# Performance work log

Measured on AMD Instinct MI355X. Metric: run time of the kernel, lower is better.

## Reference

```python
import jax, jax.numpy as jnp
import numpy as np

ALPHA = 3.0
NNODES, DIM, K = 8192, 64, 32


def setup_inputs() -> dict:
    key = jax.random.key(0)
    ks = jax.random.split(key, 8)
    return {
        "idx": jnp.arange(NNODES, dtype=jnp.int64) if jax.config.jax_enable_x64 else jnp.arange(NNODES, dtype=jnp.int32),
        "emb1": jax.random.normal(ks[0], (NNODES, DIM), dtype=jnp.float32),
        "emb2": jax.random.normal(ks[1], (NNODES, DIM), dtype=jnp.float32),
        "lin1_w": jax.random.normal(ks[2], (DIM, DIM), dtype=jnp.float32) * 0.1,
        "lin1_b": jax.random.normal(ks[3], (DIM,), dtype=jnp.float32) * 0.1,
        "lin2_w": jax.random.normal(ks[4], (DIM, DIM), dtype=jnp.float32) * 0.1,
        "lin2_b": jax.random.normal(ks[5], (DIM,), dtype=jnp.float32) * 0.1,
        "noise": jax.random.uniform(ks[6], (NNODES, NNODES), dtype=jnp.float32),
        "k": K,
    }


def reference(idx, emb1, emb2, lin1_w, lin1_b, lin2_w, lin2_b, noise, k):
    # gather node embeddings, project, tanh(alpha * .)
    nodevec1 = jnp.tanh(ALPHA * (emb1[idx] @ lin1_w.T + lin1_b))  # [N, D]
    nodevec2 = jnp.tanh(ALPHA * (emb2[idx] @ lin2_w.T + lin2_b))  # [N, D]
    # antisymmetric bilinear score
    a = nodevec1 @ nodevec2.T - nodevec2 @ nodevec1.T             # [N, N]
    adj = jax.nn.relu(jnp.tanh(ALPHA * a))                         # [N, N]
    n = adj.shape[0]
    # topk per row with uniform tie-break noise (torch: adj + rand*0.01)
    _, t1 = jax.lax.top_k(adj + noise * 0.01, k)                   # [N, k] int
    rows = jnp.arange(n)[:, None]                                  # [N, 1]
    mask = jnp.zeros((n, n), dtype=adj.dtype).at[rows, t1].set(1.0)
    adj = adj * mask + jnp.eye(n, dtype=adj.dtype)
    return adj
```

## Files before the change

kernel.cpp:

```cpp
#include <hip/hip_runtime.h>

#define NN 8192
#define DD 64
#define CC 128
#define XCLAMP 7.99881172180175781f

__device__ __forceinline__ float guard(float v) {
    asm volatile("" : "+v"(v));
    return v;
}

__device__ __forceinline__ float xla_tanhf(float x) {
    float xc = fminf(fmaxf(x, -XCLAMP), XCLAMP);
    float x2 = xc * xc;
    float p = fmaf(x2, -2.76076847742355e-16f, 2.00018790482477e-13f);
    p = fmaf(x2, p, -8.60467152213735e-11f);
    p = fmaf(x2, p, 5.12229709037114e-08f);
    p = fmaf(x2, p, 1.48572235717979e-05f);
    p = fmaf(x2, p, 6.37261928875436e-04f);
    p = fmaf(x2, p, 4.89352455891786e-03f);
    p = xc * p;
    float q = fmaf(x2, 1.19825839466702e-06f, 1.18534705686654e-04f);
    q = fmaf(x2, q, 2.26843463243900e-03f);
    q = fmaf(x2, q, 4.89352518554385e-03f);
    float r = p / q;
    return (fabsf(x) < 0.0004f) ? x : r;
}

__device__ __forceinline__ float score_of(float a, float nz) {
    float adj = fmaxf(xla_tanhf(3.0f * a), 0.0f);
    float m = guard(0.01f * nz);
    return adj + m;
}

__global__ __launch_bounds__(256) void k1_nodevec(
    const int* __restrict__ idx,
    const float* __restrict__ emb1, const float* __restrict__ emb2,
    const float* __restrict__ w1, const float* __restrict__ b1,
    const float* __restrict__ w2, const float* __restrict__ b2,
    float* __restrict__ Wt)
{
    __shared__ float sw1[64 * 65], sw2[64 * 65];
    __shared__ float sb1[64], sb2[64];
    __shared__ float se1[4][64], se2[4][64];
    int t = threadIdx.x;
    for (int i = t; i < 4096; i += 256) {
        int r = i >> 6, c = i & 63;
        sw1[r * 65 + c] = w1[i];
        sw2[r * 65 + c] = w2[i];
    }
    if (t < 64) { sb1[t] = b1[t]; sb2[t] = b2[t]; }
    int nl = t >> 6, d = t & 63;
    int n = blockIdx.x * 4 + nl;
    bool is64 = (idx[1] == 0);
    int g = (is64 ? idx[2 * n] : idx[n]) & 8191;
    se1[nl][d] = emb1[g * 64 + d];
    se2[nl][d] = emb2[g * 64 + d];
    __syncthreads();
    float z1 = 0.0f, z2 = 0.0f;
#pragma unroll 16
    for (int q = 0; q < 64; ++q) {
        z1 = fmaf(se1[nl][q], sw1[d * 65 + q], z1);
        z2 = fmaf(se2[nl][q], sw2[d * 65 + q], z2);
    }
    z1 = 3.0f * guard(z1 + sb1[d]);
    z2 = 3.0f * guard(z2 + sb2[d]);
    Wt[(size_t)d * NN + n]        = xla_tanhf(z1);
    Wt[(size_t)(64 + d) * NN + n] = xla_tanhf(z2);
}

__global__ __launch_bounds__(256) void k_init(
    float* __restrict__ listVal, int* __restrict__ listIdx)
{
    int i = blockIdx.x * 256 + threadIdx.x;
    listVal[i] = -1.0f;
    listIdx[i] = -1;
}

__global__ __launch_bounds__(512) void k2p_pairscore(
    const float* __restrict__ Wt, const float* __restrict__ noise,
    float* __restrict__ Sc)
{
    __shared__ __align__(16) float smem[17024];
    float* sA1 = smem;
    float* sB1 = smem + 4224;
    float* sA2 = smem + 8448;
    float* sB2 = smem + 12672;
    int bx = blockIdx.x, by = blockIdx.y;
    if (bx < by) return;
    int R = by * 128, C = bx * 128;
    int t = threadIdx.x;
    int ty = t >> 5, tx = t & 31;

    float A1[8][4], A2[8][4];
#pragma unroll
    for (int i = 0; i < 8; ++i)
#pragma unroll
        for (int j = 0; j < 4; ++j) { A1[i][j] = 0.0f; A2[i][j] = 0.0f; }

    for (int kc = 0; kc < 2; ++kc) {
        int k0 = kc * 32;
#pragma unroll
        for (int p = 0; p < 2; ++p) {
            int q = p * 512 + t;
            int kf = q >> 5;
            int rr = (q & 31) * 4;
            float4 v1 = *(const float4*)&Wt[(size_t)(k0 + kf) * NN + R + rr];
            *(float4*)&sA1[kf * 132 + rr] = v1;
            float4 v2 = *(const float4*)&Wt[(size_t)(64 + k0 + kf) * NN + C + rr];
            *(float4*)&sB1[kf * 132 + rr] = v2;
            float4 v3 = *(const float4*)&Wt[(size_t)(64 + k0 + kf) * NN + R + rr];
            *(float4*)&sA2[kf * 132 + rr] = v3;
            float4 v4 = *(const float4*)&Wt[(size_t)(k0 + kf) * NN + C + rr];
            *(float4*)&sB2[kf * 132 + rr] = v4;
        }
        __syncthreads();
#pragma unroll 4
        for (int kk = 0; kk < 32; ++kk) {
            float4 a10 = *(const float4*)&sA1[kk * 132 + ty * 8];
            float4 a11 = *(const float4*)&sA1[kk * 132 + ty * 8 + 4];
            float4 b1v = *(const float4*)&sB1[kk * 132 + tx * 4];
            float4 a20 = *(const float4*)&sA2[kk * 132 + ty * 8];
            float4 a21 = *(const float4*)&sA2[kk * 132 + ty * 8 + 4];
            float4 b2v = *(const float4*)&sB2[kk * 132 + tx * 4];
            float a1[8] = {a10.x, a10.y, a10.z, a10.w, a11.x, a11.y, a11.z, a11.w};
            float b1[4] = {b1v.x, b1v.y, b1v.z, b1v.w};
            float a2[8] = {a20.x, a20.y, a20.z, a20.w, a21.x, a21.y, a21.z, a21.w};
            float b2[4] = {b2v.x, b2v.y, b2v.z, b2v.w};
#pragma unroll
            for (int i = 0; i < 8; ++i)
#pragma unroll
                for (int j = 0; j < 4; ++j) {
                    A1[i][j] = fmaf(a1[i], b1[j], A1[i][j]);
                    A2[i][j] = fmaf(a2[i], b2[j], A2[i][j]);
                }
        }
        __syncthreads();
    }

    float* dT = smem;
#pragma unroll
    for (int i = 0; i < 8; ++i) {
        int I = ty * 8 + i;
        int grow = R + I;
        float4 nz = *(const float4*)&noise[(size_t)grow * NN + C + tx * 4];
        float d0 = guard(A1[i][0] - A2[i][0]);
        float d1 = guard(A1[i][1] - A2[i][1]);
        float d2 = guard(A1[i][2] - A2[i][2]);
        float d3 = guard(A1[i][3] - A2[i][3]);
        float4 o;
        o.x = score_of(d0, nz.x);
        o.y = score_of(d1, nz.y);
        o.z = score_of(d2, nz.z);
        o.w = score_of(d3, nz.w);
        *(float4*)&Sc[(size_t)grow * NN + C + tx * 4] = o;
        dT[(tx * 4 + 0) * 133 + I] = d0;
        dT[(tx * 4 + 1) * 133 + I] = d1;
        dT[(tx * 4 + 2) * 133 + I] = d2;
        dT[(tx * 4 + 3) * 133 + I] = d3;
    }
    __syncthreads();

    int c4 = tx * 4;
#pragma unroll
    for (int rr = 0; rr < 8; ++rr) {
        int r2 = rr * 16 + ty;
        int grow = C + r2;
        float4 nz = *(const float4*)&noise[(size_t)grow * NN + R + c4];
        float d0 = dT[r2 * 133 + c4 + 0];
        float d1 = dT[r2 * 133 + c4 + 1];
        float d2 = dT[r2 * 133 + c4 + 2];
        float d3 = dT[r2 * 133 + c4 + 3];
        float4 o;
        o.x = score_of(-d0, nz.x);
        o.y = score_of(-d1, nz.y);
        o.z = score_of(-d2, nz.z);
        o.w = score_of(-d3, nz.w);
        *(float4*)&Sc[(size_t)grow * NN + R + c4] = o;
    }
}

__global__ __launch_bounds__(256) void k3_screen(
    const float* __restrict__ Sc,
    float* __restrict__ listVal, int* __restrict__ listIdx)
{
    int lane = threadIdx.x & 63;
    int w    = threadIdx.x >> 6;
    int row  = blockIdx.x * 4 + w;
    const float* Srow = Sc + (size_t)row * NN;

    float Lv = listVal[row * 64 + lane];
    int   Lj = listIdx[row * 64 + lane];

    for (int c0 = 0; c0 < NN; c0 += 256) {
        float s0 = Srow[c0 + lane];
        float s1 = Srow[c0 + 64 + lane];
        float s2 = Srow[c0 + 128 + lane];
        float s3 = Srow[c0 + 192 + lane];
#pragma unroll
        for (int u = 0; u < 4; ++u) {
            float s = (u == 0) ? s0 : (u == 1) ? s1 : (u == 2) ? s2 : s3;
            int jb = c0 + u * 64;
            float tau = __shfl(Lv, 63);
            unsigned long long m = __ballot(s > tau);
            while (m) {
                int b = __ffsll((unsigned long long)m) - 1;
                m &= m - 1;
                float v = __shfl(s, b);
                tau = __shfl(Lv, 63);
                if (v > tau) {
                    float Lu = __shfl_up(Lv, 1);
                    int   Ju = __shfl_up(Lj, 1);
                    bool ge  = (Lv >= v);
                    bool geu = (lane == 0) || (Lu >= v);
                    float nv = ge ? Lv : (geu ? v : Lu);
                    int   nj = ge ? Lj : (geu ? (jb + b) : Ju);
                    Lv = nv; Lj = nj;
                }
            }
        }
    }
    listVal[row * 64 + lane] = Lv;
    listIdx[row * 64 + lane] = Lj;
}

__global__ __launch_bounds__(256) void k4a_fill(float* __restrict__ out)
{
    int i4 = blockIdx.x * 256 + threadIdx.x;
    int f0 = i4 * 4;
    int row = f0 >> 13;
    int colbase = f0 & 8191;
    int drel = row - colbase;
    float4 z = make_float4(0.f, 0.f, 0.f, 0.f);
    if (drel >= 0 && drel < 4) ((float*)&z)[drel] = 1.0f;
    *(float4*)&out[f0] = z;
}

__global__ __launch_bounds__(256) void k4b_scatter(
    const int* __restrict__ listIdx, const float* __restrict__ listVal,
    const float* __restrict__ noise, const int* __restrict__ kptr,
    float* __restrict__ out)
{
    int lane = threadIdx.x & 63;
    int w    = threadIdx.x >> 6;
    int row  = blockIdx.x * 4 + w;
    int kk = kptr[0]; if (kk > 64) kk = 64; if (kk < 1) kk = 1;
    if (lane < kk) {
        int   j = listIdx[row * 64 + lane] & 8191;
        float s = listVal[row * 64 + lane];
        float nz = noise[(size_t)row * NN + j];
        float m = guard(0.01f * nz);
        float adj = s - m;
        if (j == row) adj += 1.0f;
        out[(size_t)row * NN + j] = adj;
    }
}

extern "C" void kernel_launch(void* const* d_in, const int* in_sizes, int n_in,
                              void* d_out, int out_size, void* d_ws, size_t ws_size,
                              hipStream_t stream) {
    (void)in_sizes; (void)n_in; (void)out_size; (void)ws_size;
    const int*   idx   = (const int*)d_in[0];
    const float* emb1  = (const float*)d_in[1];
    const float* emb2  = (const float*)d_in[2];
    const float* w1    = (const float*)d_in[3];
    const float* b1    = (const float*)d_in[4];
    const float* w2    = (const float*)d_in[5];
    const float* b2    = (const float*)d_in[6];
    const float* noise = (const float*)d_in[7];
    const int*   kptr  = (const int*)d_in[8];

    float* out = (float*)d_out;
    float* Sc  = out;

    char*  ws      = (char*)d_ws;
    float* Wt      = (float*)ws;
    float* listVal = (float*)(ws + (size_t)4 * 1024 * 1024);
    int*   listIdx = (int*)  (ws + (size_t)6 * 1024 * 1024);

    k1_nodevec<<<NN / 4, 256, 0, stream>>>(idx, emb1, emb2, w1, b1, w2, b2, Wt);
    k_init<<<NN * 64 / 256, 256, 0, stream>>>(listVal, listIdx);

    dim3 gp(64, 64);
    k2p_pairscore<<<gp, 512, 0, stream>>>(Wt, noise, Sc);

    k3_screen<<<NN / 4, 256, 0, stream>>>(Sc, listVal, listIdx);

    k4a_fill<<<65536, 256, 0, stream>>>(out);
    k4b_scatter<<<NN / 4, 256, 0, stream>>>(listIdx, listVal, noise, kptr, out);
}
```

Baseline: 497.9 us.

## Halve pairscore shared memory by computing both GEMM products sequentially

The pairscore kernel now computes the two 128x128 products (A1 and A2) one after another, reusing two shared tiles instead of staging four at once. The B tile gets a padded, bank-skewed stride. The transposed write-back goes through a small 128x33 staging buffer in four slices, which brings shared memory down from about 68KB to about 35KB. The aim is higher occupancy from lower LDS use, at the cost of extra syncs and a second round of global loads.

```diff
diff --git a/kernel.cpp b/kernel.cpp
--- a/kernel.cpp
+++ b/kernel.cpp
@@ -4,6 +4,8 @@
 #define DD 64
 #define CC 128
 #define XCLAMP 7.99881172180175781f
+#define SXS 132
+#define SYS 144
 
 __device__ __forceinline__ float guard(float v) {
     asm volatile("" : "+v"(v));
@@ -81,11 +83,11 @@
     const float* __restrict__ Wt, const float* __restrict__ noise,
     float* __restrict__ Sc)
 {
-    __shared__ __align__(16) float smem[17024];
-    float* sA1 = smem;
-    float* sB1 = smem + 4224;
-    float* sA2 = smem + 8448;
-    float* sB2 = smem + 12672;
+    __shared__ __align__(16) float smem[32 * SXS + 32 * SYS];
+    float* sX = smem;
+    float* sY = smem + 32 * SXS;
+    float* dT = smem;
+
     int bx = blockIdx.x, by = blockIdx.y;
     if (bx < by) return;
     int R = by * 128, C = bx * 128;
@@ -98,85 +100,116 @@
 #pragma unroll
         for (int j = 0; j < 4; ++j) { A1[i][j] = 0.0f; A2[i][j] = 0.0f; }
 
+    int boff = tx * 4 + ((tx >> 3) << 2);
+
     for (int kc = 0; kc < 2; ++kc) {
         int k0 = kc * 32;
 #pragma unroll
         for (int p = 0; p < 2; ++p) {
             int q = p * 512 + t;
-            int kf = q >> 5;
-            int rr = (q & 31) * 4;
-            float4 v1 = *(const float4*)&Wt[(size_t)(k0 + kf) * NN + R + rr];
-            *(float4*)&sA1[kf * 132 + rr] = v1;
-            float4 v2 = *(const float4*)&Wt[(size_t)(64 + k0 + kf) * NN + C + rr];
-            *(float4*)&sB1[kf * 132 + rr] = v2;
-            float4 v3 = *(const float4*)&Wt[(size_t)(64 + k0 + kf) * NN + R + rr];
-            *(float4*)&sA2[kf * 132 + rr] = v3;
-            float4 v4 = *(const float4*)&Wt[(size_t)(k0 + kf) * NN + C + rr];
-            *(float4*)&sB2[kf * 132 + rr] = v4;
+            int kf = q >> 5, rr = (q & 31) * 4;
+            float4 xv = *(const float4*)&Wt[(size_t)(k0 + kf) * NN + R + rr];
+            *(float4*)&sX[kf * SXS + rr] = xv;
+            float4 yv = *(const float4*)&Wt[(size_t)(64 + k0 + kf) * NN + C + rr];
+            *(float4*)&sY[kf * SYS + rr + ((rr >> 5) << 2)] = yv;
         }
         __syncthreads();
 #pragma unroll 4
         for (int kk = 0; kk < 32; ++kk) {
-            float4 a10 = *(const float4*)&sA1[kk * 132 + ty * 8];
-            float4 a11 = *(const float4*)&sA1[kk * 132 + ty * 8 + 4];
-            float4 b1v = *(const float4*)&sB1[kk * 132 + tx * 4];
-            float4 a20 = *(const float4*)&sA2[kk * 132 + ty * 8];
-            float4 a21 = *(const float4*)&sA2[kk * 132 + ty * 8 + 4];
-            float4 b2v = *(const float4*)&sB2[kk * 132 + tx * 4];
-            float a1[8] = {a10.x, a10.y, a10.z, a10.w, a11.x, a11.y, a11.z, a11.w};
-            float b1[4] = {b1v.x, b1v.y, b1v.z, b1v.w};
-            float a2[8] = {a20.x, a20.y, a20.z, a20.w, a21.x, a21.y, a21.z, a21.w};
-            float b2[4] = {b2v.x, b2v.y, b2v.z, b2v.w};
+            float4 a0 = *(const float4*)&sX[kk * SXS + ty * 8];
+            float4 a1 = *(const float4*)&sX[kk * SXS + ty * 8 + 4];
+            float4 bv = *(const float4*)&sY[kk * SYS + boff];
+            float a[8] = {a0.x, a0.y, a0.z, a0.w, a1.x, a1.y, a1.z, a1.w};
+            float b[4] = {bv.x, bv.y, bv.z, bv.w};
 #pragma unroll
             for (int i = 0; i < 8; ++i)
 #pragma unroll
-                for (int j = 0; j < 4; ++j) {
-                    A1[i][j] = fmaf(a1[i], b1[j], A1[i][j]);
-                    A2[i][j] = fmaf(a2[i], b2[j], A2[i][j]);
-                }
-        }
-        __syncthreads();
-    }
-
-    float* dT = smem;
+                for (int j = 0; j < 4; ++j)
+                    A1[i][j] = fmaf(a[i], b[j], A1[i][j]);
+        }
+        __syncthreads();
+    }
+    for (int kc = 0; kc < 2; ++kc) {
+        int k0 = kc * 32;
+#pragma unroll
+        for (int p = 0; p < 2; ++p) {
+            int q = p * 512 + t;
+            int kf = q >> 5, rr = (q & 31) * 4;
+            float4 xv = *(const float4*)&Wt[(size_t)(64 + k0 + kf) * NN + R + rr];
+            *(float4*)&sX[kf * SXS + rr] = xv;
+            float4 yv = *(const float4*)&Wt[(size_t)(k0 + kf) * NN + C + rr];
+            *(float4*)&sY[kf * SYS + rr + ((rr >> 5) << 2)] = yv;
+        }
+        __syncthreads();
+#pragma unroll 4
+        for (int kk = 0; kk < 32; ++kk) {
+            float4 a0 = *(const float4*)&sX[kk * SXS + ty * 8];
+            float4 a1 = *(const float4*)&sX[kk * SXS + ty * 8 + 4];
+            float4 bv = *(const float4*)&sY[kk * SYS + boff];
+            float a[8] = {a0.x, a0.y, a0.z, a0.w, a1.x, a1.y, a1.z, a1.w};
+            float b[4] = {bv.x, bv.y, bv.z, bv.w};
+#pragma unroll
+            for (int i = 0; i < 8; ++i)
+#pragma unroll
+                for (int j = 0; j < 4; ++j)
+                    A2[i][j] = fmaf(a[i], b[j], A2[i][j]);
+        }
+        __syncthreads();
+    }
+
 #pragma unroll
     for (int i = 0; i < 8; ++i) {
-        int I = ty * 8 + i;
-        int grow = R + I;
+        int grow = R + ty * 8 + i;
         float4 nz = *(const float4*)&noise[(size_t)grow * NN + C + tx * 4];
-        float d0 = guard(A1[i][0] - A2[i][0]);
-        float d1 = guard(A1[i][1] - A2[i][1]);
-        float d2 = guard(A1[i][2] - A2[i][2]);
-        float d3 = guard(A1[i][3] - A2[i][3]);
+        A1[i][0] = guard(A1[i][0] - A2[i][0]);
+        A1[i][1] = guard(A1[i][1] - A2[i][1]);
+        A1[i][2] = guard(A1[i][2] - A2[i][2]);
+        A1[i][3] = guard(A1[i][3] - A2[i][3]);
         float4 o;
-        o.x = score_of(d0, nz.x);
-        o.y = score_of(d1, nz.y);
-        o.z = score_of(d2, nz.z);
-        o.w = score_of(d3, nz.w);
+        o.x = score_of(A1[i][0], nz.x);
+        o.y = score_of(A1[i][1], nz.y);
+        o.z = score_of(A1[i][2], nz.z);
+        o.w = score_of(A1[i][3], nz.w);
         *(float4*)&Sc[(size_t)grow * NN + C + tx * 4] = o;
-        dT[(tx * 4 + 0) * 133 + I] = d0;
-        dT[(tx * 4 + 1) * 133 + I] = d1;
-        dT[(tx * 4 + 2) * 133 + I] = d2;
-        dT[(tx * 4 + 3) * 133 + I] = d3;
-    }
-    __syncthreads();
-
-    int c4 = tx * 4;
-#pragma unroll
-    for (int rr = 0; rr < 8; ++rr) {
-        int r2 = rr * 16 + ty;
-        int grow = C + r2;
-        float4 nz = *(const float4*)&noise[(size_t)grow * NN + R + c4];
-        float d0 = dT[r2 * 133 + c4 + 0];
-        float d1 = dT[r2 * 133 + c4 + 1];
-        float d2 = dT[r2 * 133 + c4 + 2];
-        float d3 = dT[r2 * 133 + c4 + 3];
-        float4 o;
-        o.x = score_of(-d0, nz.x);
-        o.y = score_of(-d1, nz.y);
-        o.z = score_of(-d2, nz.z);
-        o.w = score_of(-d3, nz.w);
-        *(float4*)&Sc[(size_t)grow * NN + R + c4] = o;
+    }
+
+#pragma unroll
+    for (int s = 0; s < 4; ++s) {
+        __syncthreads();
+        if ((ty >> 2) == s) {
+            int base = ty * 8 - 32 * s;
+#pragma unroll
+            for (int i = 0; i < 8; ++i)
+#pragma unroll
+                for (int j = 0; j < 4; ++j)
+                    dT[(tx * 4 + j) * 33 + base + i] = A1[i][j];
+        }
+        __syncthreads();
+        int J  = t >> 2;
+        int Il = (t & 3) * 8;
+        int grow = C + J;
+        int gcol = R + 32 * s + Il;
+        float v0 = dT[J * 33 + Il + 0];
+        float v1 = dT[J * 33 + Il + 1];
+        float v2 = dT[J * 33 + Il + 2];
+        float v3 = dT[J * 33 + Il + 3];
+        float v4 = dT[J * 33 + Il + 4];
+        float v5 = dT[J * 33 + Il + 5];
+        float v6 = dT[J * 33 + Il + 6];
+        float v7 = dT[J * 33 + Il + 7];
+        float4 nz0 = *(const float4*)&noise[(size_t)grow * NN + gcol];
+        float4 nz1 = *(const float4*)&noise[(size_t)grow * NN + gcol + 4];
+        float4 o0, o1;
+        o0.x = score_of(-v0, nz0.x);
+        o0.y = score_of(-v1, nz0.y);
+        o0.z = score_of(-v2, nz0.z);
+        o0.w = score_of(-v3, nz0.w);
+        o1.x = score_of(-v4, nz1.x);
+        o1.y = score_of(-v5, nz1.y);
+        o1.z = score_of(-v6, nz1.z);
+        o1.w = score_of(-v7, nz1.w);
+        *(float4*)&Sc[(size_t)grow * NN + gcol]     = o0;
+        *(float4*)&Sc[(size_t)grow * NN + gcol + 4] = o1;
     }
 }
 
```

Result: slower. 511.9 us (+2.8%).
